# Kernel tuning notes

Measured on AMD Instinct MI355X. Metric: run time of the kernel, lower is better.

## Reference

```python
import jax, jax.numpy as jnp
import numpy as np

F4_E2M1_MAX = 6.0
F8E4M3_MAX = 448.0
E4M3_EPS = 0.015625  # torch.finfo(float8_e4m3fn).tiny = 2**-6
BLOCK = 16
KE2M1 = jnp.array([0.0, 0.5, 1.0, 1.5, 2.0, 3.0, 4.0, 6.0], dtype=jnp.float32)


def round_to_e4m3(x):
    # emulate cast to float8_e4m3fn and back (round-to-nearest-even)
    return x.astype(jnp.float8_e4m3fn).astype(jnp.float32)


def fp4_121_positive(x):
    step1 = jnp.round(2.0 * x) / 2.0   # subnormal-ish region [0,2): step 0.5
    step2 = jnp.round(x)               # [2,4): step 1
    step3 = 2.0 * jnp.round(x / 2.0)   # [4,6]: step 2
    return jnp.where(x < 2.0, step1, jnp.where(x < 4.0, step2, step3))


def cast_to_fp4(x):
    return jnp.sign(x) * fp4_121_positive(jnp.abs(x))


def unpack_fp4_from_uint8(a, m, n):
    # a: int-typed tensor holding byte values in [0,256); two fp4 codes per byte
    high = (a.reshape(-1) >> 4) & 0xF
    low = a.reshape(-1) & 0xF
    combined = jnp.stack((low, high), axis=1).reshape(m, n)  # interleave low,high
    signs = (combined & 8) != 0
    abs_idx = combined & 7
    return KE2M1[abs_idx] * jnp.where(signs, -1.0, 1.0)


def dequant_nvfp4_packed(data_lp, out_scales, per_tensor_scale):
    m, half_n = data_lp.shape
    n = half_n * 2
    data_hp = unpack_fp4_from_uint8(data_lp, m, n)           # [m, n] float32
    scale_fp = out_scales / per_tensor_scale                  # [m, n/16]
    data_hp = data_hp.reshape(m, -1, BLOCK) * scale_fp.reshape(m, -1, 1)
    return data_hp.reshape(m, n)


def qdq_nvfp4(x):
    m, n = x.shape
    tensor_amax = jnp.max(jnp.abs(x))
    pts = jnp.clip(tensor_amax / F8E4M3_MAX, E4M3_EPS, F8E4M3_MAX)  # per-tensor scale
    xb = x.reshape(m, -1, BLOCK)
    block_scale = jnp.max(jnp.abs(xb), axis=-1) / F4_E2M1_MAX       # [m, n/16]
    scaled_bs = round_to_e4m3(jnp.clip(block_scale / pts, E4M3_EPS, F8E4M3_MAX))
    total_scale = pts * scaled_bs                                   # [m, n/16]
    data_scaled = jnp.clip(xb / total_scale[..., None], -F4_E2M1_MAX, F4_E2M1_MAX)
    data_lp = cast_to_fp4(data_scaled)                              # unpacked fp4 values
    # dequant: out_scales / (1/pts) == scaled_bs * pts == total_scale
    return (data_lp * total_scale[..., None]).reshape(m, n)


def setup_inputs() -> dict:
    key = jax.random.key(0)
    k1, k2, k3 = jax.random.split(key, 3)
    M, K, N = 16384, 2048, 2048  # tokens, in_features, out_features
    x = jax.random.normal(k1, (M, K), dtype=jnp.float32)
    weight_packed = jax.random.randint(k2, (N, K // 2), 0, 256, dtype=jnp.int32)
    # fp8-representable positive block scales
    weight_scale = round_to_e4m3(jax.random.uniform(k3, (N, K // 16), dtype=jnp.float32,
                                                    minval=0.05, maxval=1.0))
    weight_global_scale = jnp.ones((1,), dtype=jnp.float32)
    return {"x": x, "weight_packed": weight_packed,
            "weight_scale": weight_scale, "weight_global_scale": weight_global_scale}


def reference(x, weight_packed, weight_scale, weight_global_scale):
    hp_weight = dequant_nvfp4_packed(weight_packed, weight_scale, weight_global_scale)
    x_dq = qdq_nvfp4(x)
    return x_dq @ hp_weight.T
```

## Files before the change

### kernel.cpp

```cpp
#include <hip/hip_runtime.h>

typedef unsigned short u16;
typedef unsigned int u32;
typedef __attribute__((ext_vector_type(8))) short short8;
typedef __attribute__((ext_vector_type(4))) float floatx4;

static constexpr int M = 16384, N = 2048, K = 2048;


__device__ inline u16 f32_to_bf16(float x) {
    u32 u = __float_as_uint(x);
    u += 0x7FFFu + ((u >> 16) & 1u);
    return (u16)(u >> 16);
}

__device__ inline float e4m3_rne(float x) {
    u32 u = __float_as_uint(x);
    u += 0x7FFFFu + ((u >> 20) & 1u);
    u &= 0xFFF00000u;
    return __uint_as_float(u);
}

__device__ inline float fp4_dec(u32 c) {
    u32 e = (c >> 1) & 3u;
    float m = (float)(c & 1u);
    float v = e ? (2.0f + m) * (float)(1u << e) * 0.25f : 0.5f * m;
    return (c & 8u) ? -v : v;
}

__device__ inline float fp4_round_mag(float a) {
    if (a < 2.0f) return rintf(2.0f * a) * 0.5f;
    if (a < 4.0f) return rintf(a);
    return 2.0f * rintf(a * 0.5f);
}

__device__ inline float pts_from_amax(float amax) {
    return fminf(fmaxf(amax / 448.0f, 0.015625f), 448.0f);
}


__global__ void amax_part(const float4* __restrict__ x, float* __restrict__ part, int n4) {
    int idx = blockIdx.x * blockDim.x + threadIdx.x;
    int stride = gridDim.x * blockDim.x;
    float m = 0.0f;
    for (int i = idx; i < n4; i += stride) {
        float4 v = x[i];
        m = fmaxf(m, fmaxf(fmaxf(fabsf(v.x), fabsf(v.y)), fmaxf(fabsf(v.z), fabsf(v.w))));
    }
#pragma unroll
    for (int off = 32; off > 0; off >>= 1)
        m = fmaxf(m, __shfl_down(m, off));
    __shared__ float sm[4];
    if ((threadIdx.x & 63) == 0) sm[threadIdx.x >> 6] = m;
    __syncthreads();
    if (threadIdx.x == 0)
        part[blockIdx.x] = fmaxf(fmaxf(sm[0], sm[1]), fmaxf(sm[2], sm[3]));
}


__global__ void amax_fin(const float* __restrict__ part, u32* __restrict__ out) {
    int t = threadIdx.x;
    float m = fmaxf(part[t], part[t + 1024]);
#pragma unroll
    for (int off = 32; off > 0; off >>= 1)
        m = fmaxf(m, __shfl_down(m, off));
    __shared__ float sm[16];
    if ((t & 63) == 0) sm[t >> 6] = m;
    __syncthreads();
    if (t < 16) {
        m = sm[t];
#pragma unroll
        for (int off = 8; off > 0; off >>= 1)
            m = fmaxf(m, __shfl_down(m, off));
        if (t == 0) *out = __float_as_uint(m);
    }
}


static constexpr int QB = (M * K / 4) / 256;
static constexpr int DB = (N * (K / 2)) / 256;

__global__ void prep(const float4* __restrict__ x, uint2* __restrict__ aq,
                     const u32* __restrict__ amax_bits,
                     const int* __restrict__ wp, const float* __restrict__ wsc,
                     const float* __restrict__ wgs, u16* __restrict__ wq) {
    if (blockIdx.x < QB) {
        int idx = blockIdx.x * blockDim.x + threadIdx.x;
        float4 v = x[idx];

        float bm = fmaxf(fmaxf(fabsf(v.x), fabsf(v.y)), fmaxf(fabsf(v.z), fabsf(v.w)));
        bm = fmaxf(bm, __shfl_xor(bm, 1));
        bm = fmaxf(bm, __shfl_xor(bm, 2));

        float pts = pts_from_amax(__uint_as_float(*amax_bits));
        float bs = bm / 6.0f;
        float sbs = e4m3_rne(fminf(fmaxf(bs / pts, 0.015625f), 448.0f));
        float ts = pts * sbs;

        float vf[4] = {v.x, v.y, v.z, v.w};
        u16 o[4];
#pragma unroll
        for (int i = 0; i < 4; i++) {
            float s = vf[i] / ts;
            s = fminf(fmaxf(s, -6.0f), 6.0f);
            float lp = copysignf(fp4_round_mag(fabsf(s)), s);
            o[i] = f32_to_bf16(lp * sbs);
        }
        aq[idx] = *(const uint2*)o;
    } else {
        int idx = (blockIdx.x - QB) * blockDim.x + threadIdx.x;
        constexpr int Khalf = K / 2;
        int n = idx >> 10;
        int kb = idx & (Khalf - 1);
        u32 byte = (u32)wp[idx] & 0xFFu;
        float scale = wsc[(size_t)n * (K / 16) + (kb >> 3)] / wgs[0];
        float lo = fp4_dec(byte & 0xFu) * scale;
        float hi = fp4_dec((byte >> 4) & 0xFu) * scale;
        u32 out = (u32)f32_to_bf16(lo) | ((u32)f32_to_bf16(hi) << 16);
        ((u32*)wq)[idx] = out;
    }
}


#define GLDS(g, l)                                                              \
    __builtin_amdgcn_global_load_lds(                                           \
        (const __attribute__((address_space(1))) unsigned int*)(g),             \
        (__attribute__((address_space(3))) unsigned int*)(l), 16, 0, 0)

__global__ __launch_bounds__(512, 2) void gemm_bt(
    const u16* __restrict__ A, const u16* __restrict__ B,
    float* __restrict__ C, const u32* __restrict__ amax_bits)
{
    __shared__ u16 sh[2][2][2][8192];

    const int tid = threadIdx.x;
    const int w = tid >> 6, lane = tid & 63;

    const int id = blockIdx.x;
    const int xcd = id & 7;
    const int local = id >> 3;
    const int bm = xcd * 8 + (local >> 3);
    const int bn = local & 7;

    const int wm = w >> 2, wn = w & 3;
    const int r16 = lane & 15, q = lane >> 4;

    floatx4 acc[8][4] = {};

    const int swz = (r16 & 7) << 4;
    const int aoff0 = r16 * 64 + (((q * 16) ^ swz) >> 1);
    const int aoff1 = r16 * 64 + (((64 + q * 16) ^ swz) >> 1);

    const int srow8 = lane >> 3;
    const int scol = ((lane & 7) ^ srow8) * 8;
    const u16* gA[2], * gB[2];
    gA[0] = A + (size_t)(bm * 256 + (w * 2 + 0) * 8 + srow8) * K + scol;
    gA[1] = A + (size_t)(bm * 256 + (w * 2 + 1) * 8 + srow8) * K + scol;
    gB[0] = B + (size_t)(bn * 256 + (w * 2 + 0) * 8 + srow8) * K + scol;
    gB[1] = B + (size_t)(bn * 256 + (w * 2 + 1) * 8 + srow8) * K + scol;

#define STG(buf, mat, half, ktc) do {                                           \
        const u16* _s0 = ((mat) ? gB[0] : gA[0]) + (size_t)(half) * 128 * K + (ktc); \
        const u16* _s1 = ((mat) ? gB[1] : gA[1]) + (size_t)(half) * 128 * K + (ktc); \
        GLDS(_s0, &sh[buf][mat][half][w * 1024]);                               \
        GLDS(_s1, &sh[buf][mat][half][w * 1024 + 512]);                         \
    } while (0)

    short8 aF[4][2], bF[4][2];

#define RD_A(buf, Qa) do {                                                      \
        const u16* _ar = &sh[buf][0][wm][(Qa) * 4096];                          \
        _Pragma("unroll") for (int _i = 0; _i < 4; _i++) {                      \
            aF[_i][0] = *(const short8*)(_ar + _i * 1024 + aoff0);              \
            aF[_i][1] = *(const short8*)(_ar + _i * 1024 + aoff1); }            \
    } while (0)

#define RD_B(buf, Qb) do {                                                      \
        const u16* _br = &sh[buf][1][wn >> 1][(wn & 1) * 4096 + (Qb) * 2048];   \
        _Pragma("unroll") for (int _j = 0; _j < 2; _j++) {                      \
            bF[(Qb) * 2 + _j][0] = *(const short8*)(_br + _j * 1024 + aoff0);   \
            bF[(Qb) * 2 + _j][1] = *(const short8*)(_br + _j * 1024 + aoff1); } \
    } while (0)

#define MMA(Qa, Qb) do {                                                        \
        __builtin_amdgcn_sched_barrier(0);                                      \
        __builtin_amdgcn_s_barrier();                                           \
        __builtin_amdgcn_sched_barrier(0);                                      \
        __builtin_amdgcn_s_setprio(1);                                          \
        _Pragma("unroll") for (int _i = 0; _i < 4; _i++)                        \
        _Pragma("unroll") for (int _j = 0; _j < 2; _j++)                        \
        _Pragma("unroll") for (int _k = 0; _k < 2; _k++)                        \
            acc[(Qa) * 4 + _i][(Qb) * 2 + _j] =                                 \
                __builtin_amdgcn_mfma_f32_16x16x32_bf16(                        \
                    aF[_i][_k], bF[(Qb) * 2 + _j][_k],                          \
                    acc[(Qa) * 4 + _i][(Qb) * 2 + _j], 0, 0, 0);                \
        __builtin_amdgcn_s_setprio(0);                                          \
        __builtin_amdgcn_sched_barrier(0);                                      \
    } while (0)

#define ENDPH __builtin_amdgcn_s_barrier()
#define CHK4 do { asm volatile("s_waitcnt vmcnt(4)" ::: "memory");              \
                  __builtin_amdgcn_sched_barrier(0); } while (0)

    STG(0, 0, 0, 0); STG(0, 0, 1, 0);
    STG(0, 1, 0, 0); STG(0, 1, 1, 0);
    STG(1, 1, 0, 64); STG(1, 1, 1, 64);
    CHK4;
    __builtin_amdgcn_s_barrier();

#pragma unroll 1
    for (int it = 0; it < K / 128; ++it) {
        const int ktY  = (2 * it + 1) * 64;
        const int kx2  = 2 * it + 2, ky2 = 2 * it + 3;
        const int ktX2 = (kx2 <= 31 ? kx2 : 31) * 64;
        const int ktY2 = (ky2 <= 31 ? ky2 : 31) * 64;

        RD_A(0, 0); RD_B(0, 0); STG(1, 0, 0, ktY);  MMA(0, 0);       ENDPH;
        RD_B(0, 1);             STG(1, 0, 1, ktY);  MMA(0, 1);       ENDPH;
        RD_A(0, 1);             STG(0, 1, 0, ktX2); MMA(1, 1);       ENDPH;
                                STG(0, 1, 1, ktX2); MMA(1, 0); CHK4; ENDPH;
        RD_A(1, 0); RD_B(1, 0); STG(0, 0, 0, ktX2); MMA(0, 0);       ENDPH;
        RD_B(1, 1);             STG(0, 0, 1, ktX2); MMA(0, 1);       ENDPH;
        RD_A(1, 1);             STG(1, 1, 0, ktY2); MMA(1, 1);       ENDPH;
                                STG(1, 1, 1, ktY2); MMA(1, 0); CHK4; ENDPH;
    }

    asm volatile("s_waitcnt vmcnt(0)" ::: "memory");

    float pts = pts_from_amax(__uint_as_float(*amax_bits));

    float* Cb = C + (size_t)(bm * 256 + wm * 128 + q * 4) * N
                  + bn * 256 + wn * 64 + r16;
#pragma unroll
    for (int i = 0; i < 8; i++)
#pragma unroll
        for (int j = 0; j < 4; j++)
#pragma unroll
            for (int t = 0; t < 4; t++)
                Cb[(size_t)(i * 16 + t) * N + j * 16] = pts * acc[i][j][t];
}


extern "C" void kernel_launch(void* const* d_in, const int* in_sizes, int n_in,
                              void* d_out, int out_size, void* d_ws, size_t ws_size,
                              hipStream_t stream) {
    const float* x   = (const float*)d_in[0];
    const int*   wp  = (const int*)d_in[1];
    const float* wsc = (const float*)d_in[2];
    const float* wgs = (const float*)d_in[3];
    float* out = (float*)d_out;

    u32*   amax_ws = (u32*)d_ws;
    float* part    = (float*)((char*)d_ws + 64);
    u16*   aq      = (u16*)((char*)d_ws + 16384);
    u16*   wq      = aq + (size_t)M * K;

    amax_part<<<2048, 256, 0, stream>>>((const float4*)x, part, M * K / 4);
    amax_fin<<<1, 1024, 0, stream>>>(part, amax_ws);
    prep<<<QB + DB, 256, 0, stream>>>((const float4*)x, (uint2*)aq, amax_ws,
                                      wp, wsc, wgs, wq);
    gemm_bt<<<(M / 256) * (N / 256), 512, 0, stream>>>(aq, wq, out, amax_ws);
}
```

Baseline: 378.7 us.

## Move weight dequant into amax pass, split GEMM launch, merge MMA phases

Weight dequantization moves from the prep kernel into the amax partial-reduction kernel, so its memory traffic overlaps with the activation amax scan. The GEMM is launched as two half-grid kernels over the M dimension, with the block-to-tile mapping adjusted. Inside the main loop, two pairs of MMA quadrants are merged into a single barrier phase, which removes two barriers per half-iteration and issues their staging loads together. The split launch adds launch overhead and changes L2 locality, and the merged phases raise the number of loads in flight per barrier.

```diff
diff --git a/kernel.cpp b/kernel.cpp
--- a/kernel.cpp
+++ b/kernel.cpp
@@ -39,7 +39,9 @@
 }
 
 
-__global__ void amax_part(const float4* __restrict__ x, float* __restrict__ part, int n4) {
+__global__ void amax_part(const float4* __restrict__ x, float* __restrict__ part, int n4,
+                          const int* __restrict__ wp, const float* __restrict__ wsc,
+                          const float* __restrict__ wgs, u16* __restrict__ wq) {
     int idx = blockIdx.x * blockDim.x + threadIdx.x;
     int stride = gridDim.x * blockDim.x;
     float m = 0.0f;
@@ -47,6 +49,20 @@
         float4 v = x[i];
         m = fmaxf(m, fmaxf(fmaxf(fabsf(v.x), fabsf(v.y)), fmaxf(fabsf(v.z), fabsf(v.w))));
     }
+
+    float ginv = wgs[0];
+#pragma unroll
+    for (int g = 0; g < 4; g++) {
+        int i = idx + g * 524288;
+        int n = i >> 10;
+        int kb = i & 1023;
+        u32 byte = (u32)wp[i] & 0xFFu;
+        float scale = wsc[(size_t)n * (K / 16) + (kb >> 3)] / ginv;
+        float lo = fp4_dec(byte & 0xFu) * scale;
+        float hi = fp4_dec((byte >> 4) & 0xFu) * scale;
+        ((u32*)wq)[i] = (u32)f32_to_bf16(lo) | ((u32)f32_to_bf16(hi) << 16);
+    }
+
 #pragma unroll
     for (int off = 32; off > 0; off >>= 1)
         m = fmaxf(m, __shfl_down(m, off));
@@ -78,47 +94,31 @@
 
 
 static constexpr int QB = (M * K / 4) / 256;
-static constexpr int DB = (N * (K / 2)) / 256;
 
 __global__ void prep(const float4* __restrict__ x, uint2* __restrict__ aq,
-                     const u32* __restrict__ amax_bits,
-                     const int* __restrict__ wp, const float* __restrict__ wsc,
-                     const float* __restrict__ wgs, u16* __restrict__ wq) {
-    if (blockIdx.x < QB) {
-        int idx = blockIdx.x * blockDim.x + threadIdx.x;
-        float4 v = x[idx];
-
-        float bm = fmaxf(fmaxf(fabsf(v.x), fabsf(v.y)), fmaxf(fabsf(v.z), fabsf(v.w)));
-        bm = fmaxf(bm, __shfl_xor(bm, 1));
-        bm = fmaxf(bm, __shfl_xor(bm, 2));
-
-        float pts = pts_from_amax(__uint_as_float(*amax_bits));
-        float bs = bm / 6.0f;
-        float sbs = e4m3_rne(fminf(fmaxf(bs / pts, 0.015625f), 448.0f));
-        float ts = pts * sbs;
-
-        float vf[4] = {v.x, v.y, v.z, v.w};
-        u16 o[4];
-#pragma unroll
-        for (int i = 0; i < 4; i++) {
-            float s = vf[i] / ts;
-            s = fminf(fmaxf(s, -6.0f), 6.0f);
-            float lp = copysignf(fp4_round_mag(fabsf(s)), s);
-            o[i] = f32_to_bf16(lp * sbs);
-        }
-        aq[idx] = *(const uint2*)o;
-    } else {
-        int idx = (blockIdx.x - QB) * blockDim.x + threadIdx.x;
-        constexpr int Khalf = K / 2;
-        int n = idx >> 10;
-        int kb = idx & (Khalf - 1);
-        u32 byte = (u32)wp[idx] & 0xFFu;
-        float scale = wsc[(size_t)n * (K / 16) + (kb >> 3)] / wgs[0];
-        float lo = fp4_dec(byte & 0xFu) * scale;
-        float hi = fp4_dec((byte >> 4) & 0xFu) * scale;
-        u32 out = (u32)f32_to_bf16(lo) | ((u32)f32_to_bf16(hi) << 16);
-        ((u32*)wq)[idx] = out;
-    }
+                     const u32* __restrict__ amax_bits) {
+    int idx = blockIdx.x * blockDim.x + threadIdx.x;
+    float4 v = x[idx];
+
+    float bm = fmaxf(fmaxf(fabsf(v.x), fabsf(v.y)), fmaxf(fabsf(v.z), fabsf(v.w)));
+    bm = fmaxf(bm, __shfl_xor(bm, 1));
+    bm = fmaxf(bm, __shfl_xor(bm, 2));
+
+    float pts = pts_from_amax(__uint_as_float(*amax_bits));
+    float bs = bm / 6.0f;
+    float sbs = e4m3_rne(fminf(fmaxf(bs / pts, 0.015625f), 448.0f));
+    float ts = pts * sbs;
+
+    float vf[4] = {v.x, v.y, v.z, v.w};
+    u16 o[4];
+#pragma unroll
+    for (int i = 0; i < 4; i++) {
+        float s = vf[i] / ts;
+        s = fminf(fmaxf(s, -6.0f), 6.0f);
+        float lp = copysignf(fp4_round_mag(fabsf(s)), s);
+        o[i] = f32_to_bf16(lp * sbs);
+    }
+    aq[idx] = *(const uint2*)o;
 }
 
 
@@ -129,7 +129,7 @@
 
 __global__ __launch_bounds__(512, 2) void gemm_bt(
     const u16* __restrict__ A, const u16* __restrict__ B,
-    float* __restrict__ C, const u32* __restrict__ amax_bits)
+    float* __restrict__ C, const u32* __restrict__ amax_bits, int bm_base)
 {
     __shared__ u16 sh[2][2][2][8192];
 
@@ -139,7 +139,7 @@
     const int id = blockIdx.x;
     const int xcd = id & 7;
     const int local = id >> 3;
-    const int bm = xcd * 8 + (local >> 3);
+    const int bm = bm_base + xcd * 4 + (local >> 3);
     const int bn = local & 7;
 
     const int wm = w >> 2, wn = w & 3;
@@ -182,23 +182,23 @@
             bF[(Qb) * 2 + _j][1] = *(const short8*)(_br + _j * 1024 + aoff1); } \
     } while (0)
 
-#define MMA(Qa, Qb) do {                                                        \
-        __builtin_amdgcn_sched_barrier(0);                                      \
-        __builtin_amdgcn_s_barrier();                                           \
-        __builtin_amdgcn_sched_barrier(0);                                      \
-        __builtin_amdgcn_s_setprio(1);                                          \
+#define MMAQ(Qa, Qb)                                                            \
         _Pragma("unroll") for (int _i = 0; _i < 4; _i++)                        \
         _Pragma("unroll") for (int _j = 0; _j < 2; _j++)                        \
         _Pragma("unroll") for (int _k = 0; _k < 2; _k++)                        \
             acc[(Qa) * 4 + _i][(Qb) * 2 + _j] =                                 \
                 __builtin_amdgcn_mfma_f32_16x16x32_bf16(                        \
                     aF[_i][_k], bF[(Qb) * 2 + _j][_k],                          \
-                    acc[(Qa) * 4 + _i][(Qb) * 2 + _j], 0, 0, 0);                \
-        __builtin_amdgcn_s_setprio(0);                                          \
-        __builtin_amdgcn_sched_barrier(0);                                      \
-    } while (0)
-
-#define ENDPH __builtin_amdgcn_s_barrier()
+                    acc[(Qa) * 4 + _i][(Qb) * 2 + _j], 0, 0, 0)
+
+#define BAR do { __builtin_amdgcn_sched_barrier(0);                             \
+                 __builtin_amdgcn_s_barrier();                                  \
+                 __builtin_amdgcn_sched_barrier(0); } while (0)
+#define PRIO1 __builtin_amdgcn_s_setprio(1)
+#define PRIO0 do { __builtin_amdgcn_s_setprio(0);                               \
+                   __builtin_amdgcn_sched_barrier(0); } while (0)
+#define ENDPH do { __builtin_amdgcn_s_barrier();                                \
+                   __builtin_amdgcn_sched_barrier(0); } while (0)
 #define CHK4 do { asm volatile("s_waitcnt vmcnt(4)" ::: "memory");              \
                   __builtin_amdgcn_sched_barrier(0); } while (0)
 
@@ -215,14 +215,18 @@
         const int ktX2 = (kx2 <= 31 ? kx2 : 31) * 64;
         const int ktY2 = (ky2 <= 31 ? ky2 : 31) * 64;
 
-        RD_A(0, 0); RD_B(0, 0); STG(1, 0, 0, ktY);  MMA(0, 0);       ENDPH;
-        RD_B(0, 1);             STG(1, 0, 1, ktY);  MMA(0, 1);       ENDPH;
-        RD_A(0, 1);             STG(0, 1, 0, ktX2); MMA(1, 1);       ENDPH;
-                                STG(0, 1, 1, ktX2); MMA(1, 0); CHK4; ENDPH;
-        RD_A(1, 0); RD_B(1, 0); STG(0, 0, 0, ktX2); MMA(0, 0);       ENDPH;
-        RD_B(1, 1);             STG(0, 0, 1, ktX2); MMA(0, 1);       ENDPH;
-        RD_A(1, 1);             STG(1, 1, 0, ktY2); MMA(1, 1);       ENDPH;
-                                STG(1, 1, 1, ktY2); MMA(1, 0); CHK4; ENDPH;
+        RD_A(0, 0); RD_B(0, 0); STG(1, 0, 0, ktY);
+        BAR; PRIO1; MMAQ(0, 0); PRIO0; ENDPH;
+        RD_B(0, 1); STG(1, 0, 1, ktY);
+        BAR; PRIO1; MMAQ(0, 1); PRIO0; ENDPH;
+        RD_A(0, 1); STG(0, 1, 0, ktX2); STG(0, 1, 1, ktX2);
+        BAR; PRIO1; MMAQ(1, 1); MMAQ(1, 0); PRIO0; CHK4; ENDPH;
+        RD_A(1, 0); RD_B(1, 0); STG(0, 0, 0, ktX2);
+        BAR; PRIO1; MMAQ(0, 0); PRIO0; ENDPH;
+        RD_B(1, 1); STG(0, 0, 1, ktX2);
+        BAR; PRIO1; MMAQ(0, 1); PRIO0; ENDPH;
+        RD_A(1, 1); STG(1, 1, 0, ktY2); STG(1, 1, 1, ktY2);
+        BAR; PRIO1; MMAQ(1, 1); MMAQ(1, 0); PRIO0; CHK4; ENDPH;
     }
 
     asm volatile("s_waitcnt vmcnt(0)" ::: "memory");
@@ -255,9 +259,10 @@
     u16*   aq      = (u16*)((char*)d_ws + 16384);
     u16*   wq      = aq + (size_t)M * K;
 
-    amax_part<<<2048, 256, 0, stream>>>((const float4*)x, part, M * K / 4);
+    amax_part<<<2048, 256, 0, stream>>>((const float4*)x, part, M * K / 4,
+                                        wp, wsc, wgs, wq);
     amax_fin<<<1, 1024, 0, stream>>>(part, amax_ws);
-    prep<<<QB + DB, 256, 0, stream>>>((const float4*)x, (uint2*)aq, amax_ws,
-                                      wp, wsc, wgs, wq);
-    gemm_bt<<<(M / 256) * (N / 256), 512, 0, stream>>>(aq, wq, out, amax_ws);
-}
+    prep<<<QB, 256, 0, stream>>>((const float4*)x, (uint2*)aq, amax_ws);
+    gemm_bt<<<256, 512, 0, stream>>>(aq, wq, out, amax_ws, 0);
+    gemm_bt<<<256, 512, 0, stream>>>(aq, wq, out, amax_ws, 32);
+}
```

After: 385.2 us. No clear change (+1.7%).
